# Kernel optimization log

Measured on AMD Instinct MI355X. Metric: run time of the kernel, lower is better.

Reference implementation:

```python
import jax, jax.numpy as jnp
import numpy as np

FIRE_RATE = 0.5
ANGLE = 0.0


def _kernels(angle):
    dx = np.outer([1, 2, 1], [-1, 0, 1]) / 8.0
    dy = dx.T
    dlap = np.array([[1, 2, 1], [2, -12, 2], [1, 2, 1]]) / 8.0
    dlap2 = np.array([[0, 1, 0], [1, -4, 1], [0, 1, 0]]) / 8.0
    c = np.cos(angle * np.pi / 180.0)
    s = np.sin(angle * np.pi / 180.0)
    w1 = c * dx - s * dy
    w2 = s * dx + c * dy
    return [jnp.asarray(k, jnp.float32) for k in (w1, w2, dlap, dlap2)]


def _dwconv(x, k):
    # x: [B,H,W,C], k: [3,3] applied depthwise (same kernel every channel)
    C = x.shape[-1]
    rhs = jnp.broadcast_to(k[:, :, None, None], (3, 3, 1, C))
    return jax.lax.conv_general_dilated(
        x, rhs, window_strides=(1, 1), padding='SAME',
        dimension_numbers=('NHWC', 'HWIO', 'NHWC'), feature_group_count=C)


def _alive(x):
    # 3x3 max-pool (stride 1, SAME) over alpha channel (index 3) > 0.1
    a = jax.lax.reduce_window(x[..., 3:4], -jnp.inf, jax.lax.max,
                              (1, 3, 3, 1), (1, 1, 1, 1), 'SAME')
    return a > 0.1


def _update(x, W0, b0, W1, key):
    pre_life = _alive(x)                                  # [B,H,W,1] bool
    ks = _kernels(ANGLE)
    y = jnp.concatenate([x] + [_dwconv(x, k) for k in ks], axis=-1)  # [B,H,W,5C]
    h = jax.nn.relu(y @ W0 + b0)                          # [B,H,W,hidden]
    d = h @ W1                                            # [B,H,W,C]
    stoch = (jax.random.uniform(key, d.shape[:3] + (1,)) > FIRE_RATE).astype(d.dtype)
    x = x + d * stoch
    life = (pre_life & _alive(x)).astype(x.dtype)
    return x * life


def setup_inputs() -> dict:
    key = jax.random.key(0)
    k1, k2, k3, k4 = jax.random.split(key, 4)
    B, H, W, C, HID = 8, 256, 256, 16, 128
    return {
        'x': jax.random.normal(k1, (B, H, W, C), jnp.float32),
        'W0': jax.random.normal(k2, (5 * C, HID), jnp.float32) * 0.05,
        'b0': jax.random.normal(k3, (HID,), jnp.float32) * 0.05,
        'W1': jax.random.normal(k4, (HID, C), jnp.float32) * 0.05,
        'steps': 2,
    }


def reference(x, W0, b0, W1, steps):
    base = jax.random.key(42)
    for step in range(steps):
        x = _update(x, W0, b0, W1, jax.random.fold_in(base, step))
    return x
```

## Files before the change

### kernel.cpp

```cpp
#include <hip/hip_runtime.h>
#include <stdint.h>

#define BB 8
#define HH 256
#define WW 256
#define CC 16
#define HID 128
#define NPIX (BB*HH*WW)
#define MTILE 64
#define NBLK (NPIX/MTILE)

typedef _Float16 h8 __attribute__((ext_vector_type(8)));
typedef __fp16   fp16v2 __attribute__((ext_vector_type(2)));
typedef float    f4 __attribute__((ext_vector_type(4)));

#define YPK_HI     0
#define YPK_MID    3328
#define HS_OFF     0
#define ALPHA5_OFF 6656
#define LIFE_OFF   6996
#define CTR_OFF    8704
#define FIRE_OFF   9984
#define LDS_DW     10048

__host__ __device__ __forceinline__ uint32_t rotl32(uint32_t x, int r) {
  return (x << r) | (x >> (32 - r));
}

__host__ __device__ inline void threefry2x32(uint32_t k0, uint32_t k1,
                                             uint32_t x0, uint32_t x1,
                                             uint32_t& o0, uint32_t& o1) {
  const uint32_t ks2 = k0 ^ k1 ^ 0x1BD11BDAu;
  x0 += k0; x1 += k1;
#define TF_R4(a,b,c,d) \
  x0 += x1; x1 = rotl32(x1,(a)); x1 ^= x0; \
  x0 += x1; x1 = rotl32(x1,(b)); x1 ^= x0; \
  x0 += x1; x1 = rotl32(x1,(c)); x1 ^= x0; \
  x0 += x1; x1 = rotl32(x1,(d)); x1 ^= x0;
  TF_R4(13,15,26,6)   x0 += k1;  x1 += ks2 + 1u;
  TF_R4(17,29,16,24)  x0 += ks2; x1 += k0 + 2u;
  TF_R4(13,15,26,6)   x0 += k0;  x1 += k1 + 3u;
  TF_R4(17,29,16,24)  x0 += k1;  x1 += ks2 + 4u;
  TF_R4(13,15,26,6)   x0 += ks2; x1 += k0 + 5u;
#undef TF_R4
  o0 = x0; o1 = x1;
}

__device__ __forceinline__ void split2(float a, float b, uint32_t& hi, uint32_t& mid) {
  _Float16 ha = (_Float16)a, hb = (_Float16)b;
  union { _Float16 h[2]; uint32_t u; } ph;
  ph.h[0] = ha; ph.h[1] = hb; hi = ph.u;
  float ra = a - (float)ha, rb = b - (float)hb;
  union { fp16v2 h; uint32_t u; } pu;
  pu.h = __builtin_amdgcn_cvt_pkrtz(ra, rb);
  mid = pu.u;
}

__global__ __launch_bounds__(256)
void prep_frags(const float* __restrict__ W0g, const float* __restrict__ W1g,
                uint32_t* __restrict__ W0F, uint32_t* __restrict__ W1F) {
  const int tid = blockIdx.x * 256 + threadIdx.x;
  for (int idx = tid; idx < 6144; idx += gridDim.x * 256) {
    const int r = idx & 3, l = (idx >> 2) & 63, ks = (idx >> 8) % 3, n = idx / 768;
    const int g = l >> 4, c = l & 15;
    const int k0 = 32 * ks + 8 * g + 2 * r;
    const int hid = 16 * n + c;
    const float a = (k0     < 80) ? W0g[k0 * HID + hid]       : 0.f;
    const float b = (k0 + 1 < 80) ? W0g[(k0 + 1) * HID + hid] : 0.f;
    uint32_t hi, mid; split2(a, b, hi, mid);
    W0F[(size_t)(((n * 3 + ks) * 2 + 0) * 64 + l) * 4 + r] = hi;
    W0F[(size_t)(((n * 3 + ks) * 2 + 1) * 64 + l) * 4 + r] = mid;
  }
  for (int idx = tid; idx < 1024; idx += gridDim.x * 256) {
    const int r = idx & 3, l = (idx >> 2) & 63, ks = idx >> 8;
    const int g = l >> 4, c = l & 15;
    float va[2];
#pragma unroll
    for (int h = 0; h < 2; ++h) {
      const int khat = 2 * g + 16 * (r & 1) + 8 * h + (r >> 1);
      va[h] = W1g[(size_t)(32 * ks + khat) * CC + c];
    }
    uint32_t hi, mid; split2(va[0], va[1], hi, mid);
    W1F[(size_t)((ks * 2 + 0) * 64 + l) * 4 + r] = hi;
    W1F[(size_t)((ks * 2 + 1) * 64 + l) * 4 + r] = mid;
  }
}

__global__ __launch_bounds__(256, 4)
void step_fused(const float* __restrict__ xin,
                const uint32_t* __restrict__ W0F,
                const uint32_t* __restrict__ W1F,
                const float* __restrict__ b0g,
                const float* __restrict__ aPrev,
                const unsigned char* __restrict__ mPrev,
                float* __restrict__ xn,
                float* __restrict__ alpha_out,
                unsigned char* __restrict__ prelife,
                uint32_t k0, uint32_t k1, int apply_life) {
  __shared__ uint32_t LDSU[LDS_DW];
  float* const LDSF = (float*)LDSU;

  const int t    = threadIdx.x;
  const int blk  = blockIdx.x;
  const int lane = t & 63;
  const int w    = __builtin_amdgcn_readfirstlane(t >> 6);
  const int g    = lane >> 4;
  const int c15  = lane & 15;

  uint4 BH[2][2], BM[2][2];
#pragma unroll
  for (int nl = 0; nl < 2; ++nl) {
    const int n = 2 * w + nl;
    BH[0][nl] = *(const uint4*)(W0F + (size_t)(((n * 3 + 0) * 2 + 0) * 64 + lane) * 4);
    BM[0][nl] = *(const uint4*)(W0F + (size_t)(((n * 3 + 0) * 2 + 1) * 64 + lane) * 4);
  }
  const float bv0 = b0g[16 * (2 * w + 0) + c15];
  const float bv1 = b0g[16 * (2 * w + 1) + c15];

  const int base_ = blk * MTILE;
  const int bi    = base_ >> 16;
  const int rc    = base_ & 0xFFFF;
  const int ic    = rc >> 8;
  const int jc0   = rc & 0xFF;

  if (apply_life) {
    const float* ap = aPrev + (size_t)bi * (HH * WW);
    for (int it = t; it < 340; it += 256) {
      const int r = it / 68, c = it - r * 68;
      const int ii = ic - 2 + r, jj = jc0 - 2 + c;
      float v = 0.f;
      if ((unsigned)ii < (unsigned)HH && (unsigned)jj < (unsigned)WW)
        v = ap[ii * WW + jj];
      LDSF[ALPHA5_OFF + it] = v;
    }
    __syncthreads();
    if (t < 198) {
      const int r = t / 66, xx = t - r * 66;
      const float* a0 = &LDSF[ALPHA5_OFF + r * 68 + xx];
      const float m0 = fmaxf(fmaxf(a0[0],   a0[1]),   a0[2]);
      const float m1 = fmaxf(fmaxf(a0[68],  a0[69]),  a0[70]);
      const float m2 = fmaxf(fmaxf(a0[136], a0[137]), a0[138]);
      const float mm = fmaxf(fmaxf(m0, m1), m2);
      const int ii = ic - 1 + r, jj = jc0 - 1 + xx;
      int pl = 0;
      if ((unsigned)ii < (unsigned)HH && (unsigned)jj < (unsigned)WW)
        pl = mPrev[(size_t)bi * (HH * WW) + ii * WW + jj];
      LDSF[LIFE_OFF + t] = (pl && mm > 0.1f) ? 1.0f : 0.0f;
    }
    __syncthreads();
  }

  const int px  = t >> 2;
  const int c4  = (t & 3) * 4;
  const int gpx = base_ + px;
  const int jc  = jc0 + px;

  const float DXW[3][3] = {{-0.125f, 0.0f, 0.125f},
                           {-0.25f,  0.0f, 0.25f },
                           {-0.125f, 0.0f, 0.125f}};
  const float DYW[3][3] = {{-0.125f, -0.25f, -0.125f},
                           { 0.0f,    0.0f,   0.0f  },
                           { 0.125f,  0.25f,  0.125f}};
  const float LPW[3][3] = {{0.125f, 0.25f, 0.125f},
                           {0.25f, -1.5f,  0.25f },
                           {0.125f, 0.25f, 0.125f}};
  const float L2W[3][3] = {{0.0f,   0.125f, 0.0f  },
                           {0.125f, -0.5f,  0.125f},
                           {0.0f,   0.125f, 0.0f  }};

  float ctr[4] = {0,0,0,0};
  float adx[4] = {0,0,0,0};
  float ady[4] = {0,0,0,0};
  float alp[4] = {0,0,0,0};
  float al2[4] = {0,0,0,0};
  float amax = 0.0f;

  const float* xb = xin + (size_t)bi * (HH * WW * CC);
#pragma unroll
  for (int di = -1; di <= 1; ++di) {
#pragma unroll
    for (int dj = -1; dj <= 1; ++dj) {
      const int ii = ic + di, jj = jc + dj;
      const bool ok = ((unsigned)ii < (unsigned)HH) && ((unsigned)jj < (unsigned)WW);
      float4 p = make_float4(0.f, 0.f, 0.f, 0.f);
      if (ok) p = *(const float4*)(xb + ((size_t)(ii * WW + jj) * CC + c4));
      if (apply_life) {
        const float lf = LDSF[LIFE_OFF + (di + 1) * 66 + (px + dj + 1)];
        p.x *= lf; p.y *= lf; p.z *= lf; p.w *= lf;
      }
      const float wdx = DXW[di+1][dj+1], wdy = DYW[di+1][dj+1];
      const float wlp = LPW[di+1][dj+1], wl2 = L2W[di+1][dj+1];
      const float pv[4] = {p.x, p.y, p.z, p.w};
#pragma unroll
      for (int q = 0; q < 4; ++q) {
        if (di == 0 && dj == 0) ctr[q] = pv[q];
        if (wdx != 0.f) adx[q] = fmaf(pv[q], wdx, adx[q]);
        if (wdy != 0.f) ady[q] = fmaf(pv[q], wdy, ady[q]);
        if (wlp != 0.f) alp[q] = fmaf(pv[q], wlp, alp[q]);
        if (wl2 != 0.f) al2[q] = fmaf(pv[q], wl2, al2[q]);
      }
      if (c4 == 0) amax = fmaxf(amax, p.w);
    }
  }

  {
    const int q2 = c4 >> 1;
#define WRYPK(grp, A) do { \
    uint32_t h0_, m0_, h1_, m1_; \
    split2(A[0], A[1], h0_, m0_); split2(A[2], A[3], h1_, m1_); \
    const int kk_ = 8 * (grp) + q2; \
    *(uint2*)&LDSU[YPK_HI  + px * 52 + kk_] = make_uint2(h0_, h1_); \
    *(uint2*)&LDSU[YPK_MID + px * 52 + kk_] = make_uint2(m0_, m1_); \
  } while (0)
    WRYPK(0, ctr); WRYPK(1, adx); WRYPK(2, ady); WRYPK(3, alp); WRYPK(4, al2);
#undef WRYPK
  }
#pragma unroll
  for (int j = 0; j < 4; ++j) {
    const int pos = t * 4 + j;
    const int plane = pos >> 9, rem = pos & 511;
    LDSU[plane * 3328 + (rem >> 3) * 52 + 40 + (rem & 7)] = 0u;
  }
  *(f4*)&LDSU[CTR_OFF + px * 20 + c4] = (f4){ctr[0], ctr[1], ctr[2], ctr[3]};
  if (c4 == 0) prelife[gpx] = (amax > 0.1f) ? 1 : 0;
  if (t < 64) {
    uint32_t lo, hi2;
    threefry2x32(k0, k1, 0u, (uint32_t)(base_ + t), lo, hi2);
    const uint32_t bits = lo ^ hi2;
    const float u = __uint_as_float((bits >> 9) | 0x3f800000u) - 1.0f;
    LDSF[FIRE_OFF + t] = (u > 0.5f) ? 1.0f : 0.0f;
  }

  __syncthreads();

  f4 C1[4][2];
#pragma unroll
  for (int m = 0; m < 4; ++m) {
    C1[m][0] = (f4){bv0, bv0, bv0, bv0};
    C1[m][1] = (f4){bv1, bv1, bv1, bv1};
  }

#define LOADB(par, kss) do { \
  _Pragma("unroll") for (int nl_ = 0; nl_ < 2; ++nl_) { \
    const int n_ = 2 * w + nl_; \
    BH[par][nl_] = *(const uint4*)(W0F + (size_t)(((n_ * 3 + (kss)) * 2 + 0) * 64 + lane) * 4); \
    BM[par][nl_] = *(const uint4*)(W0F + (size_t)(((n_ * 3 + (kss)) * 2 + 1) * 64 + lane) * 4); \
  } } while (0)

  const int abase = c15 * 52 + 4 * g;
#pragma unroll
  for (int ks = 0; ks < 3; ++ks) {
    if (ks == 0) LOADB(1, 1);
    if (ks == 1) LOADB(0, 2);
    const int cur = ks & 1;
#pragma unroll
    for (int m = 0; m < 4; ++m) {
      const uint4 uh = *(const uint4*)&LDSU[YPK_HI  + abase + m * 832 + 16 * ks];
      const uint4 um = *(const uint4*)&LDSU[YPK_MID + abase + m * 832 + 16 * ks];
      const h8 ah = __builtin_bit_cast(h8, uh);
      const h8 am = __builtin_bit_cast(h8, um);
#pragma unroll
      for (int nl = 0; nl < 2; ++nl) {
        const h8 bh = __builtin_bit_cast(h8, BH[cur][nl]);
        const h8 bm = __builtin_bit_cast(h8, BM[cur][nl]);
        C1[m][nl] = __builtin_amdgcn_mfma_f32_16x16x32_f16(ah, bh, C1[m][nl], 0, 0, 0);
        C1[m][nl] = __builtin_amdgcn_mfma_f32_16x16x32_f16(am, bh, C1[m][nl], 0, 0, 0);
        C1[m][nl] = __builtin_amdgcn_mfma_f32_16x16x32_f16(ah, bm, C1[m][nl], 0, 0, 0);
      }
    }
  }
#undef LOADB

  __syncthreads();

#pragma unroll
  for (int m = 0; m < 4; ++m)
#pragma unroll
    for (int nl = 0; nl < 2; ++nl) {
      f4 hv = C1[m][nl];
      hv.x = fmaxf(hv.x, 0.f); hv.y = fmaxf(hv.y, 0.f);
      hv.z = fmaxf(hv.z, 0.f); hv.w = fmaxf(hv.w, 0.f);
      const int hid = 16 * (2 * w + nl) + c15;
      *(f4*)&LDSU[HS_OFF + hid * 68 + 16 * m + 4 * g] = hv;
    }

  uint4 W1H[4], W1M[4];
#pragma unroll
  for (int ks = 0; ks < 4; ++ks) {
    W1H[ks] = *(const uint4*)(W1F + (size_t)((ks * 2 + 0) * 64 + lane) * 4);
    W1M[ks] = *(const uint4*)(W1F + (size_t)((ks * 2 + 1) * 64 + lane) * 4);
  }

  __syncthreads();

  f4 C2 = (f4){0.f, 0.f, 0.f, 0.f};
  const int A2 = 136 * g + 16 * w + c15;
#pragma unroll
  for (int ks = 0; ks < 4; ++ks) {
    uint32_t ph[4], pm[4];
#pragma unroll
    for (int r = 0; r < 4; ++r) {
      const int K0 = 16 * (r & 1) + (r >> 1);
      const float a = LDSF[A2 + 68 * (32 * ks + K0)];
      const float b = LDSF[A2 + 68 * (32 * ks + K0 + 8)];
      split2(a, b, ph[r], pm[r]);
    }
    const uint4 uh = make_uint4(ph[0], ph[1], ph[2], ph[3]);
    const uint4 um = make_uint4(pm[0], pm[1], pm[2], pm[3]);
    const h8 bh = __builtin_bit_cast(h8, uh);
    const h8 bm = __builtin_bit_cast(h8, um);
    const h8 ah = __builtin_bit_cast(h8, W1H[ks]);
    const h8 am = __builtin_bit_cast(h8, W1M[ks]);
    C2 = __builtin_amdgcn_mfma_f32_16x16x32_f16(ah, bh, C2, 0, 0, 0);
    C2 = __builtin_amdgcn_mfma_f32_16x16x32_f16(am, bh, C2, 0, 0, 0);
    C2 = __builtin_amdgcn_mfma_f32_16x16x32_f16(ah, bm, C2, 0, 0, 0);
  }

  {
    const int pxt  = 16 * w + c15;
    const int gpx2 = base_ + pxt;
    const f4 ctr4 = *(const f4*)&LDSU[CTR_OFF + pxt * 20 + 4 * g];
    const float fire01 = LDSF[FIRE_OFF + pxt];
    f4 xv;
    xv.x = fmaf(C2.x, fire01, ctr4.x);
    xv.y = fmaf(C2.y, fire01, ctr4.y);
    xv.z = fmaf(C2.z, fire01, ctr4.z);
    xv.w = fmaf(C2.w, fire01, ctr4.w);
    *(f4*)&xn[(size_t)gpx2 * CC + 4 * g] = xv;
    if (g == 0) alpha_out[gpx2] = xv.w;
  }
}

__global__ __launch_bounds__(256)
void life_final(float* __restrict__ out,
                const float* __restrict__ alpha,
                const unsigned char* __restrict__ prelife) {
  const int idx = blockIdx.x * 256 + threadIdx.x;
  const int b  = idx >> 16;
  const int ij = idx & 0xFFFF;
  const int i  = ij >> 8;
  const int j  = ij & 0xFF;

  const float* ab = alpha + (size_t)b * (HH * WW);
  float amax = 0.0f;
#pragma unroll
  for (int di = -1; di <= 1; ++di) {
    const int ii = i + di;
    if ((unsigned)ii >= (unsigned)HH) continue;
#pragma unroll
    for (int dj = -1; dj <= 1; ++dj) {
      const int jj = j + dj;
      if ((unsigned)jj >= (unsigned)WW) continue;
      amax = fmaxf(amax, ab[(size_t)ii * WW + jj]);
    }
  }
  const bool life = (prelife[idx] != 0) && (amax > 0.1f);
  if (!life) {
    const float4 z = make_float4(0.0f, 0.0f, 0.0f, 0.0f);
    float4* dst = (float4*)(out + (size_t)idx * CC);
    dst[0] = z; dst[1] = z; dst[2] = z; dst[3] = z;
  }
}

extern "C" void kernel_launch(void* const* d_in, const int* in_sizes, int n_in,
                              void* d_out, int out_size, void* d_ws, size_t ws_size,
                              hipStream_t stream) {
  (void)in_sizes; (void)n_in; (void)out_size; (void)ws_size;
  const float* x  = (const float*)d_in[0];
  const float* W0 = (const float*)d_in[1];
  const float* b0 = (const float*)d_in[2];
  const float* W1 = (const float*)d_in[3];
  float* out = (float*)d_out;

  float* xn = (float*)d_ws;
  float* alphaA = xn + (size_t)NPIX * CC;
  float* alphaB = alphaA + NPIX;
  unsigned char* maskA = (unsigned char*)(alphaB + NPIX);
  unsigned char* maskB = maskA + NPIX;
  uint32_t* W0F = (uint32_t*)(maskB + NPIX);
  uint32_t* W1F = W0F + 12288;

  prep_frags<<<24, 256, 0, stream>>>(W0, W1, W0F, W1F);

  uint32_t fk0, fk1;
  threefry2x32(0u, 42u, 0u, 0u, fk0, fk1);
  step_fused<<<NBLK, 256, 0, stream>>>(x, W0F, W1F, b0, alphaA, maskA,
                                       xn, alphaA, maskA, fk0, fk1, 0);
  threefry2x32(0u, 42u, 0u, 1u, fk0, fk1);
  step_fused<<<NBLK, 256, 0, stream>>>(xn, W0F, W1F, b0, alphaA, maskA,
                                       out, alphaB, maskB, fk0, fk1, 1);
  life_final<<<NPIX / 256, 256, 0, stream>>>(out, alphaB, maskB);
}
```

Before: 217.4 us.

## Remap stencil threads to MFMA output layout, shrink LDS, swizzle hidden tile

Stencil threads are remapped so each thread computes the same pixel and channel quad it later writes from the MFMA output. The centre value and fire mask therefore stay in registers instead of going through LDS. The hidden-activation staging buffer uses an XOR swizzle with 128-float rows to reduce bank conflicts. LDS shrinks to 32KB, occupancy is raised to 5 blocks, and apply_life becomes a template parameter. In exchange every thread now computes threefry redundantly, and the new stencil load pattern may coalesce differently.

```diff
diff --git a/kernel.cpp b/kernel.cpp
--- a/kernel.cpp
+++ b/kernel.cpp
@@ -16,12 +16,9 @@
 
 #define YPK_HI     0
 #define YPK_MID    3328
-#define HS_OFF     0
 #define ALPHA5_OFF 6656
 #define LIFE_OFF   6996
-#define CTR_OFF    8704
-#define FIRE_OFF   9984
-#define LDS_DW     10048
+#define LDS_DW     8192
 
 __host__ __device__ __forceinline__ uint32_t rotl32(uint32_t x, int r) {
   return (x << r) | (x >> (32 - r));
@@ -86,7 +83,8 @@
   }
 }
 
-__global__ __launch_bounds__(256, 4)
+template <int APPLY_LIFE>
+__global__ __launch_bounds__(256, 5)
 void step_fused(const float* __restrict__ xin,
                 const uint32_t* __restrict__ W0F,
                 const uint32_t* __restrict__ W1F,
@@ -96,7 +94,7 @@
                 float* __restrict__ xn,
                 float* __restrict__ alpha_out,
                 unsigned char* __restrict__ prelife,
-                uint32_t k0, uint32_t k1, int apply_life) {
+                uint32_t k0, uint32_t k1) {
   __shared__ uint32_t LDSU[LDS_DW];
   float* const LDSF = (float*)LDSU;
 
@@ -123,7 +121,7 @@
   const int ic    = rc >> 8;
   const int jc0   = rc & 0xFF;
 
-  if (apply_life) {
+  if constexpr (APPLY_LIFE) {
     const float* ap = aPrev + (size_t)bi * (HH * WW);
     for (int it = t; it < 340; it += 256) {
       const int r = it / 68, c = it - r * 68;
@@ -150,8 +148,8 @@
     __syncthreads();
   }
 
-  const int px  = t >> 2;
-  const int c4  = (t & 3) * 4;
+  const int px  = 16 * w + c15;
+  const int c4  = 4 * g;
   const int gpx = base_ + px;
   const int jc  = jc0 + px;
 
@@ -184,7 +182,7 @@
       const bool ok = ((unsigned)ii < (unsigned)HH) && ((unsigned)jj < (unsigned)WW);
       float4 p = make_float4(0.f, 0.f, 0.f, 0.f);
       if (ok) p = *(const float4*)(xb + ((size_t)(ii * WW + jj) * CC + c4));
-      if (apply_life) {
+      if constexpr (APPLY_LIFE) {
         const float lf = LDSF[LIFE_OFF + (di + 1) * 66 + (px + dj + 1)];
         p.x *= lf; p.y *= lf; p.z *= lf; p.w *= lf;
       }
@@ -199,12 +197,21 @@
         if (wlp != 0.f) alp[q] = fmaf(pv[q], wlp, alp[q]);
         if (wl2 != 0.f) al2[q] = fmaf(pv[q], wl2, al2[q]);
       }
-      if (c4 == 0) amax = fmaxf(amax, p.w);
-    }
-  }
-
+      if (g == 0) amax = fmaxf(amax, p.w);
+    }
+  }
+
+  float fire01;
   {
-    const int q2 = c4 >> 1;
+    uint32_t lo, hi2;
+    threefry2x32(k0, k1, 0u, (uint32_t)gpx, lo, hi2);
+    const uint32_t bits = lo ^ hi2;
+    const float u = __uint_as_float((bits >> 9) | 0x3f800000u) - 1.0f;
+    fire01 = (u > 0.5f) ? 1.0f : 0.0f;
+  }
+
+  {
+    const int q2 = g << 1;
 #define WRYPK(grp, A) do { \
     uint32_t h0_, m0_, h1_, m1_; \
     split2(A[0], A[1], h0_, m0_); split2(A[2], A[3], h1_, m1_); \
@@ -221,15 +228,7 @@
     const int plane = pos >> 9, rem = pos & 511;
     LDSU[plane * 3328 + (rem >> 3) * 52 + 40 + (rem & 7)] = 0u;
   }
-  *(f4*)&LDSU[CTR_OFF + px * 20 + c4] = (f4){ctr[0], ctr[1], ctr[2], ctr[3]};
-  if (c4 == 0) prelife[gpx] = (amax > 0.1f) ? 1 : 0;
-  if (t < 64) {
-    uint32_t lo, hi2;
-    threefry2x32(k0, k1, 0u, (uint32_t)(base_ + t), lo, hi2);
-    const uint32_t bits = lo ^ hi2;
-    const float u = __uint_as_float((bits >> 9) | 0x3f800000u) - 1.0f;
-    LDSF[FIRE_OFF + t] = (u > 0.5f) ? 1.0f : 0.0f;
-  }
+  if (g == 0) prelife[gpx] = (amax > 0.1f) ? 1 : 0;
 
   __syncthreads();
 
@@ -273,16 +272,33 @@
 
   __syncthreads();
 
-#pragma unroll
-  for (int m = 0; m < 4; ++m)
-#pragma unroll
-    for (int nl = 0; nl < 2; ++nl) {
-      f4 hv = C1[m][nl];
-      hv.x = fmaxf(hv.x, 0.f); hv.y = fmaxf(hv.y, 0.f);
-      hv.z = fmaxf(hv.z, 0.f); hv.w = fmaxf(hv.w, 0.f);
-      const int hid = 16 * (2 * w + nl) + c15;
-      *(f4*)&LDSU[HS_OFF + hid * 68 + 16 * m + 4 * g] = hv;
-    }
+  {
+    const int sg = (g & 1) << 4;
+    const int hid0 = 32 * w + c15;
+    const int hid1 = hid0 + 16;
+    const int hx00 = hid0 ^ sg,       hx01 = hid0 ^ (sg | 1);
+    const int hx02 = hid0 ^ (sg | 8), hx03 = hid0 ^ (sg | 9);
+    const int hx10 = hid1 ^ sg,       hx11 = hid1 ^ (sg | 1);
+    const int hx12 = hid1 ^ (sg | 8), hx13 = hid1 ^ (sg | 9);
+#pragma unroll
+    for (int m = 0; m < 4; ++m) {
+      const int rowb = (16 * m + 4 * g) * 128;
+      {
+        f4 hv = C1[m][0];
+        LDSF[rowb +   0 + hx00] = fmaxf(hv.x, 0.f);
+        LDSF[rowb + 128 + hx01] = fmaxf(hv.y, 0.f);
+        LDSF[rowb + 256 + hx02] = fmaxf(hv.z, 0.f);
+        LDSF[rowb + 384 + hx03] = fmaxf(hv.w, 0.f);
+      }
+      {
+        f4 hv = C1[m][1];
+        LDSF[rowb +   0 + hx10] = fmaxf(hv.x, 0.f);
+        LDSF[rowb + 128 + hx11] = fmaxf(hv.y, 0.f);
+        LDSF[rowb + 256 + hx12] = fmaxf(hv.z, 0.f);
+        LDSF[rowb + 384 + hx13] = fmaxf(hv.w, 0.f);
+      }
+    }
+  }
 
   uint4 W1H[4], W1M[4];
 #pragma unroll
@@ -294,40 +310,45 @@
   __syncthreads();
 
   f4 C2 = (f4){0.f, 0.f, 0.f, 0.f};
-  const int A2 = 136 * g + 16 * w + c15;
-#pragma unroll
-  for (int ks = 0; ks < 4; ++ks) {
-    uint32_t ph[4], pm[4];
+  {
+    const int swzr  = (c15 & 1) | ((c15 & 6) << 2);
+    const int hbase = px * 128 + 2 * g;
+    int ka[4], kb[4];
 #pragma unroll
     for (int r = 0; r < 4; ++r) {
       const int K0 = 16 * (r & 1) + (r >> 1);
-      const float a = LDSF[A2 + 68 * (32 * ks + K0)];
-      const float b = LDSF[A2 + 68 * (32 * ks + K0 + 8)];
-      split2(a, b, ph[r], pm[r]);
-    }
-    const uint4 uh = make_uint4(ph[0], ph[1], ph[2], ph[3]);
-    const uint4 um = make_uint4(pm[0], pm[1], pm[2], pm[3]);
-    const h8 bh = __builtin_bit_cast(h8, uh);
-    const h8 bm = __builtin_bit_cast(h8, um);
-    const h8 ah = __builtin_bit_cast(h8, W1H[ks]);
-    const h8 am = __builtin_bit_cast(h8, W1M[ks]);
-    C2 = __builtin_amdgcn_mfma_f32_16x16x32_f16(ah, bh, C2, 0, 0, 0);
-    C2 = __builtin_amdgcn_mfma_f32_16x16x32_f16(am, bh, C2, 0, 0, 0);
-    C2 = __builtin_amdgcn_mfma_f32_16x16x32_f16(ah, bm, C2, 0, 0, 0);
+      ka[r] = K0 ^ swzr;
+      kb[r] = (K0 + 8) ^ swzr;
+    }
+#pragma unroll
+    for (int ks = 0; ks < 4; ++ks) {
+      uint32_t ph[4], pm[4];
+#pragma unroll
+      for (int r = 0; r < 4; ++r) {
+        const float a = LDSF[hbase + 32 * ks + ka[r]];
+        const float b = LDSF[hbase + 32 * ks + kb[r]];
+        split2(a, b, ph[r], pm[r]);
+      }
+      const uint4 uh = make_uint4(ph[0], ph[1], ph[2], ph[3]);
+      const uint4 um = make_uint4(pm[0], pm[1], pm[2], pm[3]);
+      const h8 bh = __builtin_bit_cast(h8, uh);
+      const h8 bm = __builtin_bit_cast(h8, um);
+      const h8 ah = __builtin_bit_cast(h8, W1H[ks]);
+      const h8 am = __builtin_bit_cast(h8, W1M[ks]);
+      C2 = __builtin_amdgcn_mfma_f32_16x16x32_f16(ah, bh, C2, 0, 0, 0);
+      C2 = __builtin_amdgcn_mfma_f32_16x16x32_f16(am, bh, C2, 0, 0, 0);
+      C2 = __builtin_amdgcn_mfma_f32_16x16x32_f16(ah, bm, C2, 0, 0, 0);
+    }
   }
 
   {
-    const int pxt  = 16 * w + c15;
-    const int gpx2 = base_ + pxt;
-    const f4 ctr4 = *(const f4*)&LDSU[CTR_OFF + pxt * 20 + 4 * g];
-    const float fire01 = LDSF[FIRE_OFF + pxt];
     f4 xv;
-    xv.x = fmaf(C2.x, fire01, ctr4.x);
-    xv.y = fmaf(C2.y, fire01, ctr4.y);
-    xv.z = fmaf(C2.z, fire01, ctr4.z);
-    xv.w = fmaf(C2.w, fire01, ctr4.w);
-    *(f4*)&xn[(size_t)gpx2 * CC + 4 * g] = xv;
-    if (g == 0) alpha_out[gpx2] = xv.w;
+    xv.x = fmaf(C2.x, fire01, ctr[0]);
+    xv.y = fmaf(C2.y, fire01, ctr[1]);
+    xv.z = fmaf(C2.z, fire01, ctr[2]);
+    xv.w = fmaf(C2.w, fire01, ctr[3]);
+    *(f4*)&xn[(size_t)gpx * CC + c4] = xv;
+    if (g == 0) alpha_out[gpx] = xv.w;
   }
 }
 
@@ -384,10 +405,10 @@
 
   uint32_t fk0, fk1;
   threefry2x32(0u, 42u, 0u, 0u, fk0, fk1);
-  step_fused<<<NBLK, 256, 0, stream>>>(x, W0F, W1F, b0, alphaA, maskA,
-                                       xn, alphaA, maskA, fk0, fk1, 0);
+  step_fused<0><<<NBLK, 256, 0, stream>>>(x, W0F, W1F, b0, nullptr, nullptr,
+                                          xn, alphaA, maskA, fk0, fk1);
   threefry2x32(0u, 42u, 0u, 1u, fk0, fk1);
-  step_fused<<<NBLK, 256, 0, stream>>>(xn, W0F, W1F, b0, alphaA, maskA,
-                                       out, alphaB, maskB, fk0, fk1, 1);
+  step_fused<1><<<NBLK, 256, 0, stream>>>(xn, W0F, W1F, b0, alphaA, maskA,
+                                          out, alphaB, maskB, fk0, fk1);
   life_final<<<NPIX / 256, 256, 0, stream>>>(out, alphaB, maskB);
 }
```

Result: slower. 222.7 us (+2.4%).
